# Kernel optimization log

Hardware: AMD Instinct MI355X
Metric: run time of the kernel (lower is better)

The kernel has to match this reference:

```python
import jax, jax.numpy as jnp
import numpy as np

NH, NL, NPNT = 8, 4, 4          # heads, levels, points
NQ, BS, NK, D, DFFN = 100, 8, 18, 256, 1024
SPATIAL = np.array([[92, 92], [46, 46], [23, 23], [12, 12]], np.int32)
LEN_MEM = int((SPATIAL[:, 0] * SPATIAL[:, 1]).sum())  # 11253


def _layernorm(x, g, b):
    m = x.mean(-1, keepdims=True)
    v = ((x - m) ** 2).mean(-1, keepdims=True)
    return (x - m) / jnp.sqrt(v + 1e-5) * g + b


def _mha(xq, xk, xv, in_w, in_b, out_w, out_b):
    # torch nn.MultiheadAttention semantics, inputs (S, B, D)
    S, B, d = xq.shape
    dh = d // NH
    wq, wk, wv = jnp.split(in_w, 3, axis=0)
    bq, bk, bv = jnp.split(in_b, 3, axis=0)
    def proj(x, w, b):
        return (x @ w.T + b).reshape(x.shape[0], B, NH, dh).transpose(1, 2, 0, 3)
    q = proj(xq, wq, bq) * (1.0 / np.sqrt(dh))
    k = proj(xk, wk, bk)
    v = proj(xv, wv, bv)
    att = jax.nn.softmax(jnp.einsum('bhqd,bhkd->bhqk', q, k), axis=-1)
    o = jnp.einsum('bhqk,bhkd->bhqd', att, v).transpose(2, 0, 1, 3).reshape(S, B, d)
    return o @ out_w.T + out_b


def _bilinear(v_l, loc):
    # v_l: (bs,H,W,NH,dh); loc: (bs,Lq,NH,P,2) normalized [0,1]
    # matches F.grid_sample(align_corners=False, padding_mode='zeros')
    bs, H, W, nh, dh = v_l.shape
    x = loc[..., 0] * W - 0.5
    y = loc[..., 1] * H - 0.5
    x0 = jnp.floor(x); y0 = jnp.floor(y)
    lx = x - x0; ly = y - y0
    b_idx = jnp.arange(bs)[:, None, None, None]
    h_idx = jnp.arange(nh)[None, None, :, None]
    def corner(xa, ya, w):
        valid = (xa >= 0) & (xa < W) & (ya >= 0) & (ya < H)
        xi = jnp.clip(xa, 0, W - 1).astype(jnp.int32)
        yi = jnp.clip(ya, 0, H - 1).astype(jnp.int32)
        return v_l[b_idx, yi, xi, h_idx] * (w * valid)[..., None]
    return (corner(x0, y0, (1 - lx) * (1 - ly)) + corner(x0 + 1, y0, lx * (1 - ly))
            + corner(x0, y0 + 1, (1 - lx) * ly) + corner(x0 + 1, y0 + 1, lx * ly))


def _msda(q, rp, mem, pad_mask, ss, off_w, off_b, aw_w, aw_b, val_w, val_b, outp_w, outp_b):
    bs, Lq, d = q.shape
    dh = d // NH
    value = mem @ val_w.T + val_b
    value = jnp.where(pad_mask[..., None], 0.0, value).reshape(bs, -1, NH, dh)
    off = (q @ off_w.T + off_b).reshape(bs, Lq, NH, NL, NPNT, 2)
    aw = jax.nn.softmax((q @ aw_w.T + aw_b).reshape(bs, Lq, NH, NL * NPNT), -1)
    aw = aw.reshape(bs, Lq, NH, NL, NPNT)
    wh = jnp.asarray(ss[:, ::-1].copy(), jnp.float32)  # offset normalizer (W, H)
    loc = rp[:, :, None, :, None, :] + off / wh[None, None, None, :, None, :]
    out = jnp.zeros((bs, Lq, NH, dh), q.dtype)
    start = 0
    for l in range(NL):
        H, W = int(ss[l, 0]), int(ss[l, 1])
        v_l = value[:, start:start + H * W].reshape(bs, H, W, NH, dh)
        start += H * W
        samp = _bilinear(v_l, loc[:, :, :, l])          # (bs,Lq,NH,P,dh)
        out = out + (samp * aw[:, :, :, l, :, None]).sum(3)
    return out.reshape(bs, Lq, d) @ outp_w.T + outp_b


def _forward(tgt_pose, pos, ref_points, memory, w_in_w, w_in_b, w_out_w, w_out_b,
             a_in_w, a_in_b, a_out_w, a_out_b, off_w, off_b, aw_w, aw_b,
             val_w, val_b, outp_w, outp_b, wn_g, wn_b, an_g, an_b,
             n1_g, n1_b, n2_g, n2_b, l1_w, l1_b, l2_w, l2_b,
             spatial_shapes, level_start_index, padding_mask):
    ss = np.asarray(jax.device_get(spatial_shapes))
    nq, bs, nk, d = tgt_pose.shape
    # within-group self-attn over the nk keypoint tokens.
    # NOTE: with_pos_embed mutates tgt_pose in place in the torch code, so
    # q = k = v = tgt + pos and the residual also uses tgt + pos (faithful).
    t = tgt_pose + pos
    x = t.reshape(nq * bs, nk, d).transpose(1, 0, 2)   # (nk, nq*bs, d)
    a1 = _mha(x, x, x, w_in_w, w_in_b, w_out_w, w_out_b)
    t = _layernorm(t + a1.transpose(1, 0, 2).reshape(nq, bs, nk, d), wn_g, wn_b)
    # across-group self-attn over the nq groups
    x2 = t.reshape(nq, bs * nk, d)
    a2 = _mha(x2, x2, x2, a_in_w, a_in_b, a_out_w, a_out_b)
    t = _layernorm(t + a2.reshape(nq, bs, nk, d), an_g, an_b)
    # MSDeformAttn cross-attention (in-place pos add again, faithful)
    t = t + pos
    q = t.transpose(1, 0, 2, 3).reshape(bs, nq * nk, d)
    rp = jnp.swapaxes(ref_points, 0, 1)                # (bs, nq*nk, NL, 2)
    mem = jnp.swapaxes(memory, 0, 1)                   # (bs, LEN_MEM, d)
    c = _msda(q, rp, mem, padding_mask, ss, off_w, off_b, aw_w, aw_b,
              val_w, val_b, outp_w, outp_b)
    c = c.reshape(bs, nq, nk, d).transpose(1, 0, 2, 3)
    t = _layernorm(t + c, n1_g, n1_b)
    # FFN (dropout is identity in eval)
    h = jax.nn.relu(t @ l1_w.T + l1_b)
    return _layernorm(t + (h @ l2_w.T + l2_b), n2_g, n2_b)


def setup_inputs() -> dict:
    key = jax.random.key(0)
    ks = jax.random.split(key, 16)
    p = lambda k, shape: jax.random.normal(k, shape, jnp.float32) * 0.02
    lsi = np.concatenate([[0], np.cumsum(SPATIAL[:, 0] * SPATIAL[:, 1])[:-1]]).astype(np.int32)
    return {
        'tgt_pose': jax.random.normal(ks[0], (NQ, BS, NK, D), jnp.float32),
        'pos': jax.random.normal(ks[1], (NQ, BS, NK, D), jnp.float32),
        'ref_points': jax.random.uniform(ks[2], (NQ * NK, BS, NL, 2), jnp.float32),
        'memory': jax.random.normal(ks[3], (LEN_MEM, BS, D), jnp.float32),
        'w_in_w': p(ks[4], (3 * D, D)), 'w_in_b': jnp.zeros((3 * D,)),
        'w_out_w': p(ks[5], (D, D)), 'w_out_b': jnp.zeros((D,)),
        'a_in_w': p(ks[6], (3 * D, D)), 'a_in_b': jnp.zeros((3 * D,)),
        'a_out_w': p(ks[7], (D, D)), 'a_out_b': jnp.zeros((D,)),
        'off_w': p(ks[8], (NH * NL * NPNT * 2, D)),
        'off_b': jax.random.uniform(ks[9], (NH * NL * NPNT * 2,), jnp.float32, -2.0, 2.0),
        'aw_w': p(ks[10], (NH * NL * NPNT, D)), 'aw_b': jnp.zeros((NH * NL * NPNT,)),
        'val_w': p(ks[11], (D, D)), 'val_b': jnp.zeros((D,)),
        'outp_w': p(ks[12], (D, D)), 'outp_b': jnp.zeros((D,)),
        'wn_g': jnp.ones((D,)), 'wn_b': jnp.zeros((D,)),
        'an_g': jnp.ones((D,)), 'an_b': jnp.zeros((D,)),
        'n1_g': jnp.ones((D,)), 'n1_b': jnp.zeros((D,)),
        'n2_g': jnp.ones((D,)), 'n2_b': jnp.zeros((D,)),
        'l1_w': p(ks[13], (DFFN, D)), 'l1_b': jnp.zeros((DFFN,)),
        'l2_w': p(ks[14], (D, DFFN)), 'l2_b': jnp.zeros((D,)),
        'spatial_shapes': jnp.asarray(SPATIAL),
        'level_start_index': jnp.asarray(lsi),
        'padding_mask': jnp.zeros((BS, LEN_MEM), bool),
    }


def reference(tgt_pose, pos, ref_points, memory, w_in_w, w_in_b, w_out_w, w_out_b,
              a_in_w, a_in_b, a_out_w, a_out_b, off_w, off_b, aw_w, aw_b,
              val_w, val_b, outp_w, outp_b, wn_g, wn_b, an_g, an_b,
              n1_g, n1_b, n2_g, n2_b, l1_w, l1_b, l2_w, l2_b,
              spatial_shapes, level_start_index, padding_mask):
    return _forward(tgt_pose, pos, ref_points, memory, w_in_w, w_in_b, w_out_w, w_out_b,
                    a_in_w, a_in_b, a_out_w, a_out_b, off_w, off_b, aw_w, aw_b,
                    val_w, val_b, outp_w, outp_b, wn_g, wn_b, an_g, an_b,
                    n1_g, n1_b, n2_g, n2_b, l1_w, l1_b, l2_w, l2_b,
                    spatial_shapes, level_start_index, padding_mask)
```

## Files before the change

### kernel.cpp

```cpp
#include <hip/hip_runtime.h>
#include <math.h>

#define NH_ 8
#define D_ 256
#define NK_ 18
#define NQ_ 100
#define BS_ 8
#define LQ_ 1800
#define LEN_MEM_ 11253
#define NTOK_ 14400

typedef short bf16x8 __attribute__((ext_vector_type(8)));
typedef float f32x4 __attribute__((ext_vector_type(4)));
typedef unsigned short ushort;

__device__ inline ushort f2bf(float f) {
    unsigned int u = __builtin_bit_cast(unsigned int, f);
    unsigned int r = (u + 0x7fffu + ((u >> 16) & 1u)) >> 16;
    return (ushort)r;
}
__device__ inline float bf2f(unsigned int u16) {
    unsigned int i = u16 << 16;
    return __builtin_bit_cast(float, i);
}
__device__ inline int packbf2(float a, float b) {
    return (int)f2bf(a) | ((int)f2bf(b) << 16);
}

__global__ __launch_bounds__(256)
void wcvt_kernel(const float* s0, const float* s1, const float* s2, const float* s3,
                 const float* s4, const float* s5, const float* s6, const float* s7,
                 const float* s8, const float* s9, ushort* dst) {
    const int sizes[10] = {196608,65536,196608,65536,65536,32768,65536,65536,262144,262144};
    const int offs[10]  = {0,196608,262144,458752,524288,589824,622592,688128,753664,1015808};
    int ti = blockIdx.y;
    const float* s;
    switch (ti) {
        case 0: s = s0; break; case 1: s = s1; break; case 2: s = s2; break;
        case 3: s = s3; break; case 4: s = s4; break; case 5: s = s5; break;
        case 6: s = s6; break; case 7: s = s7; break; case 8: s = s8; break;
        default: s = s9; break;
    }
    int n = sizes[ti];
    int i = (blockIdx.x * 256 + threadIdx.x) * 8;
    if (i >= n) return;
    ushort* d = dst + offs[ti] + i;
    float4 f0 = *(const float4*)(s + i);
    float4 f1 = *(const float4*)(s + i + 4);
    int4 val;
    val.x = packbf2(f0.x, f0.y);
    val.y = packbf2(f0.z, f0.w);
    val.z = packbf2(f1.x, f1.y);
    val.w = packbf2(f1.z, f1.w);
    *(int4*)d = val;
}

__global__ __launch_bounds__(256)
void addcvt_kernel(const float* __restrict__ a, const float* __restrict__ b,
                   float* __restrict__ c, ushort* __restrict__ cbf, int n4) {
    int i = blockIdx.x * blockDim.x + threadIdx.x;
    if (i >= n4) return;
    float4 av = ((const float4*)a)[i];
    float4 bv = ((const float4*)b)[i];
    float4 cv;
    cv.x = av.x + bv.x; cv.y = av.y + bv.y; cv.z = av.z + bv.z; cv.w = av.w + bv.w;
    ((float4*)c)[i] = cv;
    uint2 p;
    p.x = (unsigned int)packbf2(cv.x, cv.y);
    p.y = (unsigned int)packbf2(cv.z, cv.w);
    *(uint2*)(cbf + (size_t)i * 4) = p;
}

template<int MODE, bool RELU, bool A_F32, bool OUT_BF16, int BN, int WAVES>
__global__ __launch_bounds__(WAVES * 64)
void gemmw_kernel(const void* __restrict__ Av, const ushort* __restrict__ W,
                  const float* __restrict__ bias, void* __restrict__ Cv,
                  int M, int N, const unsigned char* __restrict__ mask) {
    constexpr int K = 256;
    constexpr int NT = BN / 16;
    __shared__ ushort Ws[32 * BN * 8];
    const int tid = threadIdx.x;
    const int m0 = blockIdx.x * (WAVES * 16);
    const int n0 = blockIdx.y * BN;

    for (int c = tid; c < 32 * BN; c += WAVES * 64) {
        int kc = c & 31, n = c >> 5;
        int dst = kc * BN + (n ^ (kc & 7));
        *(int4*)(Ws + dst * 8) = *(const int4*)(W + (long)(n0 + n) * K + kc * 8);
    }
    __syncthreads();

    const int wv = tid >> 6, lane = tid & 63, fr = lane & 15, hi = lane >> 4;
    const int wm0 = m0 + wv * 16;
    int gr = wm0 + fr;
    if (gr > M - 1) gr = M - 1;
    long arow;
    if (MODE == 2) {
        int b = gr / LQ_; int lq = gr - b * LQ_;
        int q = lq / NK_; int kk = lq - q * NK_;
        arow = (long)q * (BS_ * NK_) + b * NK_ + kk;
    } else {
        arow = gr;
    }

    f32x4 acc[NT];
#pragma unroll
    for (int t = 0; t < NT; ++t) acc[t] = f32x4{0.f, 0.f, 0.f, 0.f};

    if (A_F32) {
        const float* ap = (const float*)Av + arow * (long)K + hi * 8;
        float4 p0 = *(const float4*)ap;
        float4 p1 = *(const float4*)(ap + 4);
#pragma unroll
        for (int ks = 0; ks < 8; ++ks) {
            int4 v;
            v.x = packbf2(p0.x, p0.y); v.y = packbf2(p0.z, p0.w);
            v.z = packbf2(p1.x, p1.y); v.w = packbf2(p1.z, p1.w);
            bf16x8 cur = __builtin_bit_cast(bf16x8, v);
            if (ks < 7) {
                p0 = *(const float4*)(ap + (ks + 1) * 32);
                p1 = *(const float4*)(ap + (ks + 1) * 32 + 4);
            }
            const int kc = ks * 4 + hi;
            const ushort* wb = Ws + ((kc * BN) + (fr ^ (kc & 7))) * 8;
#pragma unroll
            for (int t = 0; t < NT; ++t) {
                bf16x8 wf = *(const bf16x8*)(wb + t * 128);
                acc[t] = __builtin_amdgcn_mfma_f32_16x16x32_bf16(cur, wf, acc[t], 0, 0, 0);
            }
        }
    } else {
        const ushort* ap = (const ushort*)Av + arow * (long)K + hi * 8;
        bf16x8 afrag = *(const bf16x8*)ap;
#pragma unroll
        for (int ks = 0; ks < 8; ++ks) {
            bf16x8 cur = afrag;
            if (ks < 7) afrag = *(const bf16x8*)(ap + (ks + 1) * 32);
            const int kc = ks * 4 + hi;
            const ushort* wb = Ws + ((kc * BN) + (fr ^ (kc & 7))) * 8;
#pragma unroll
            for (int t = 0; t < NT; ++t) {
                bf16x8 wf = *(const bf16x8*)(wb + t * 128);
                acc[t] = __builtin_amdgcn_mfma_f32_16x16x32_bf16(cur, wf, acc[t], 0, 0, 0);
            }
        }
    }

#pragma unroll
    for (int r = 0; r < 4; ++r) {
        int gm = wm0 + hi * 4 + r;
        if (gm >= M) continue;
        long orow = gm;
        bool zero = false;
        if (MODE == 1) {
            if (mask && mask[(size_t)(gm & 7) * LEN_MEM_ + (gm >> 3)]) zero = true;
        } else if (MODE == 3) {
            int b = gm / LQ_; int lq = gm - b * LQ_;
            int q = lq / NK_; int kk = lq - q * NK_;
            orow = (long)q * (BS_ * NK_) + b * NK_ + kk;
        }
#pragma unroll
        for (int t = 0; t < NT; ++t) {
            int gn = n0 + t * 16 + fr;
            float v = acc[t][r] + bias[gn];
            if (RELU) v = fmaxf(v, 0.f);
            if (zero) v = 0.f;
            if (OUT_BF16) ((ushort*)Cv)[orow * (long)N + gn] = f2bf(v);
            else ((float*)Cv)[orow * (long)N + gn] = v;
        }
    }
}

template<int MODE, bool RELU, bool A_F32, bool OUT_BF16>
__global__ __launch_bounds__(256)
void gemm_kernel(const void* __restrict__ Av, const ushort* __restrict__ W,
                 const float* __restrict__ bias, void* __restrict__ Cv,
                 int M, int N, int K, const unsigned char* __restrict__ mask) {
    constexpr int AST = 72;
    __shared__ ushort As[128 * AST];
    __shared__ ushort Bs[128 * AST];
    const int m0 = blockIdx.x * 128, n0 = blockIdx.y * 128;
    const int tid = threadIdx.x;
    const int w = tid >> 6, lane = tid & 63;
    const int wr = w >> 1, wc = w & 1;
    const int fr = lane & 15, hi = lane >> 4;
    f32x4 acc[4][4];
#pragma unroll
    for (int i = 0; i < 4; ++i)
#pragma unroll
        for (int j = 0; j < 4; ++j) acc[i][j] = f32x4{0.f, 0.f, 0.f, 0.f};

    const int srow = tid >> 1, shalf = tid & 1;
    long arow = 0;
    const bool avalid = (m0 + srow) < M;
    {
        int gr = m0 + srow;
        if (gr >= M) gr = M - 1;
        arow = gr;
    }

    for (int k0 = 0; k0 < K; k0 += 64) {
        ushort* ad = As + srow * AST + shalf * 32;
        if (avalid) {
            const ushort* ap = (const ushort*)Av + arow * (long)K + k0 + shalf * 32;
#pragma unroll
            for (int i = 0; i < 4; ++i) *(int4*)(ad + i * 8) = *(const int4*)(ap + i * 8);
        } else {
            int4 z = make_int4(0, 0, 0, 0);
#pragma unroll
            for (int i = 0; i < 4; ++i) *(int4*)(ad + i * 8) = z;
        }
        {
            const ushort* wp = W + (long)(n0 + srow) * K + k0 + shalf * 32;
            ushort* bd = Bs + srow * AST + shalf * 32;
#pragma unroll
            for (int i = 0; i < 4; ++i) *(int4*)(bd + i * 8) = *(const int4*)(wp + i * 8);
        }
        __syncthreads();
#pragma unroll
        for (int kb = 0; kb < 2; ++kb) {
            bf16x8 af[4], bfr[4];
#pragma unroll
            for (int i = 0; i < 4; ++i)
                af[i] = *(const bf16x8*)(As + (wr * 64 + i * 16 + fr) * AST + kb * 32 + hi * 8);
#pragma unroll
            for (int j = 0; j < 4; ++j)
                bfr[j] = *(const bf16x8*)(Bs + (wc * 64 + j * 16 + fr) * AST + kb * 32 + hi * 8);
#pragma unroll
            for (int i = 0; i < 4; ++i)
#pragma unroll
                for (int j = 0; j < 4; ++j)
                    acc[i][j] = __builtin_amdgcn_mfma_f32_16x16x32_bf16(af[i], bfr[j], acc[i][j], 0, 0, 0);
        }
        __syncthreads();
    }

#pragma unroll
    for (int i = 0; i < 4; ++i) {
#pragma unroll
        for (int r = 0; r < 4; ++r) {
            int gm = m0 + wr * 64 + i * 16 + hi * 4 + r;
            if (gm >= M) continue;
#pragma unroll
            for (int j = 0; j < 4; ++j) {
                int gn = n0 + wc * 64 + j * 16 + fr;
                float v = acc[i][j][r] + bias[gn];
                if (RELU) v = fmaxf(v, 0.f);
                if (OUT_BF16) ((ushort*)Cv)[(long)gm * N + gn] = f2bf(v);
                else ((float*)Cv)[(long)gm * N + gn] = v;
            }
        }
    }
}

template<int S, int SP, int HPB>
__global__ __launch_bounds__(256)
void mattn_kernel(const ushort* __restrict__ qkv, ushort* __restrict__ outb,
                  int rsG, int rsS) {
    constexpr int SPk = ((SP + 31) / 32) * 32;
    constexpr int KST = 40;
    constexpr int PST = SPk + 8;
    constexpr int NT = SP / 16;
    constexpr int NB = HPB * NT;
    constexpr int HB = 8 / HPB;
    __shared__ ushort KsA[HPB * SP * KST];
    __shared__ ushort VtA[HPB * 32 * PST];
    __shared__ ushort PA [HPB * SP * PST];

    const int tid = threadIdx.x;
    const int g = blockIdx.x / HB;
    const int hbase = (blockIdx.x % HB) * HPB;

    for (int idx = tid; idx < HPB * S * 4; idx += 256) {
        int hh = idx / (S * 4); int rem = idx - hh * (S * 4);
        int j = rem >> 2, q = rem & 3;
        const ushort* base = qkv + ((size_t)g * rsG + (size_t)j * rsS) * 768 + (hbase + hh) * 32 + q * 8;
        uint4 kv = *(const uint4*)(base + 256);
        ushort* kd = KsA + hh * (SP * KST) + j * KST + q * 8;
        *(uint2*)kd = make_uint2(kv.x, kv.y);
        *(uint2*)(kd + 4) = make_uint2(kv.z, kv.w);
        uint4 vv = *(const uint4*)(base + 512);
        ushort* vt = VtA + hh * (32 * PST) + j;
        unsigned int uu[4] = {vv.x, vv.y, vv.z, vv.w};
#pragma unroll
        for (int e = 0; e < 4; ++e) {
            vt[(q * 8 + e * 2    ) * PST] = (ushort)(uu[e] & 0xffff);
            vt[(q * 8 + e * 2 + 1) * PST] = (ushort)(uu[e] >> 16);
        }
    }
    for (int idx = tid; idx < HPB * 32 * (SPk - S); idx += 256) {
        int hh = idx / (32 * (SPk - S)); int rem = idx - hh * (32 * (SPk - S));
        int d = rem / (SPk - S); int c = S + rem - d * (SPk - S);
        VtA[hh * 32 * PST + d * PST + c] = 0;
    }
    if constexpr (SPk > SP) {
        constexpr int PW = SPk - SP;
        for (int idx = tid; idx < HPB * SP * PW; idx += 256) {
            int hh = idx / (SP * PW); int rem = idx - hh * (SP * PW);
            int rrow = rem / PW; int c = SP + rem - rrow * PW;
            PA[hh * SP * PST + rrow * PST + c] = 0;
        }
    }
    __syncthreads();

    const int wv = tid >> 6, lane = tid & 63, fr = lane & 15, hi = lane >> 4;
    for (int band = wv; band < NB; band += 4) {
        const int hh = band / NT, mb = band - (band / NT) * NT;
        const int h = hbase + hh;
        const ushort* Ks = KsA + hh * (SP * KST);
        const ushort* Vt = VtA + hh * (32 * PST);
        ushort* P = PA + hh * (SP * PST);

        int sq = mb * 16 + fr; if (sq > S - 1) sq = S - 1;
        bf16x8 qf = *(const bf16x8*)(qkv + ((size_t)g * rsG + (size_t)sq * rsS) * 768 + h * 32 + hi * 8);
        f32x4 sc[NT];
#pragma unroll
        for (int t = 0; t < NT; ++t) {
            bf16x8 kf = *(const bf16x8*)(Ks + (t * 16 + fr) * KST + hi * 8);
            sc[t] = __builtin_amdgcn_mfma_f32_16x16x32_bf16(qf, kf, f32x4{0.f, 0.f, 0.f, 0.f}, 0, 0, 0);
        }
#pragma unroll
        for (int t = 0; t < NT; ++t) {
            bool valid = (t * 16 + fr) < S;
#pragma unroll
            for (int r = 0; r < 4; ++r)
                sc[t][r] = valid ? sc[t][r] * 0.17677669529663687f : -1e30f;
        }
#pragma unroll
        for (int r = 0; r < 4; ++r) {
            float m = sc[0][r];
#pragma unroll
            for (int t = 1; t < NT; ++t) m = fmaxf(m, sc[t][r]);
            m = fmaxf(m, __shfl_xor(m, 1)); m = fmaxf(m, __shfl_xor(m, 2));
            m = fmaxf(m, __shfl_xor(m, 4)); m = fmaxf(m, __shfl_xor(m, 8));
            float e[NT]; float sum = 0.f;
#pragma unroll
            for (int t = 0; t < NT; ++t) { e[t] = __expf(sc[t][r] - m); sum += e[t]; }
            sum += __shfl_xor(sum, 1); sum += __shfl_xor(sum, 2);
            sum += __shfl_xor(sum, 4); sum += __shfl_xor(sum, 8);
            float inv = 1.f / sum;
            int row = mb * 16 + hi * 4 + r;
#pragma unroll
            for (int t = 0; t < NT; ++t)
                P[row * PST + t * 16 + fr] = f2bf(e[t] * inv);
        }
        f32x4 o0 = {0.f, 0.f, 0.f, 0.f}, o1 = {0.f, 0.f, 0.f, 0.f};
#pragma unroll
        for (int kb = 0; kb < SPk / 32; ++kb) {
            bf16x8 pf = *(const bf16x8*)(P + (mb * 16 + fr) * PST + kb * 32 + hi * 8);
            bf16x8 v0 = *(const bf16x8*)(Vt + fr * PST + kb * 32 + hi * 8);
            bf16x8 v1 = *(const bf16x8*)(Vt + (16 + fr) * PST + kb * 32 + hi * 8);
            o0 = __builtin_amdgcn_mfma_f32_16x16x32_bf16(pf, v0, o0, 0, 0, 0);
            o1 = __builtin_amdgcn_mfma_f32_16x16x32_bf16(pf, v1, o1, 0, 0, 0);
        }
#pragma unroll
        for (int r = 0; r < 4; ++r) {
            int s = mb * 16 + hi * 4 + r;
            if (s < S) {
                size_t ob = ((size_t)g * rsG + (size_t)s * rsS) * 256 + h * 32;
                outb[ob + fr] = f2bf(o0[r]);
                outb[ob + 16 + fr] = f2bf(o1[r]);
            }
        }
    }
}

__global__ __launch_bounds__(256)
void addln_kernel(const float* __restrict__ base, const float* __restrict__ delta,
                  const float* __restrict__ gamma, const float* __restrict__ beta,
                  const float* __restrict__ pos,
                  float* __restrict__ out, ushort* __restrict__ obf, int M) {
    int row = blockIdx.x * 4 + (threadIdx.x >> 6);
    int lane = threadIdx.x & 63;
    if (row >= M) return;
    const float* pb = base + (size_t)row * 256;
    const float* pd = delta + (size_t)row * 256;
    float v[4]; float s = 0.f;
#pragma unroll
    for (int i = 0; i < 4; ++i) { int c = lane + i * 64; v[i] = pb[c] + pd[c]; s += v[i]; }
#pragma unroll
    for (int off = 32; off; off >>= 1) s += __shfl_xor(s, off);
    float mean = s * (1.f / 256.f);
    float var = 0.f;
#pragma unroll
    for (int i = 0; i < 4; ++i) { float d = v[i] - mean; var += d * d; }
#pragma unroll
    for (int off = 32; off; off >>= 1) var += __shfl_xor(var, off);
    var *= (1.f / 256.f);
    float rstd = rsqrtf(var + 1e-5f);
#pragma unroll
    for (int i = 0; i < 4; ++i) {
        int c = lane + i * 64;
        float o = (v[i] - mean) * rstd * gamma[c] + beta[c];
        if (pos) o += pos[(size_t)row * 256 + c];
        out[(size_t)row * 256 + c] = o;
        if (obf) obf[(size_t)row * 256 + c] = f2bf(o);
    }
}

__global__ __launch_bounds__(256)
void msda_kernel(const float* __restrict__ offb, const float* __restrict__ aw,
                 const ushort* __restrict__ val, const float* __restrict__ refp,
                 const int* __restrict__ spatial, const int* __restrict__ lsi,
                 ushort* __restrict__ samp) {
    int unit = blockIdx.x * 16 + (threadIdx.x >> 4);
    int lane = threadIdx.x & 15;
    int lbase = (threadIdx.x & 63) & 48;
    int h = unit & 7;
    int t = unit >> 3;
    int lq = t % LQ_;
    int b = t / LQ_;

    float logit = aw[((size_t)b * LQ_ + lq) * 128 + h * 16 + lane];
    float m = logit;
    m = fmaxf(m, __shfl_xor(m, 1)); m = fmaxf(m, __shfl_xor(m, 2));
    m = fmaxf(m, __shfl_xor(m, 4)); m = fmaxf(m, __shfl_xor(m, 8));
    float e = __expf(logit - m);
    float sum = e;
    sum += __shfl_xor(sum, 1); sum += __shfl_xor(sum, 2);
    sum += __shfl_xor(sum, 4); sum += __shfl_xor(sum, 8);
    float wnorm = e / sum;

    const float* offp = offb + ((size_t)b * LQ_ + lq) * 256 + h * 32;
    float2 myoff = ((const float2*)offp)[lane];

    float acc0 = 0.f, acc1 = 0.f;
#pragma unroll
    for (int lvl = 0; lvl < 4; ++lvl) {
        int H = spatial[lvl * 2], W = spatial[lvl * 2 + 1];
        int st = lsi[lvl];
        float rpx = refp[(((size_t)lq * BS_ + b) * 4 + lvl) * 2 + 0];
        float rpy = refp[(((size_t)lq * BS_ + b) * 4 + lvl) * 2 + 1];
        const ushort* vb = val + ((size_t)st * 8 + b) * 256 + h * 32 + lane * 2;
        float fW = (float)W, fH = (float)H;
#pragma unroll
        for (int p = 0; p < 4; ++p) {
            int pi = lvl * 4 + p;
            float ox = __shfl(myoff.x, lbase + pi);
            float oy = __shfl(myoff.y, lbase + pi);
            float wpt = __shfl(wnorm, lbase + pi);
            float x = rpx * fW + ox - 0.5f;
            float y = rpy * fH + oy - 0.5f;
            float x0f = floorf(x), y0f = floorf(y);
            float lx = x - x0f, ly = y - y0f;
            int x0 = (int)x0f, y0 = (int)y0f;
            int xc0 = min(max(x0, 0), W - 1), xc1 = min(max(x0 + 1, 0), W - 1);
            int yc0 = min(max(y0, 0), H - 1), yc1 = min(max(y0 + 1, 0), H - 1);
            float vx0 = (x0 >= 0 && x0 < W) ? 1.f : 0.f;
            float vx1 = (x0 >= -1 && x0 + 1 < W) ? 1.f : 0.f;
            float vy0 = (y0 >= 0 && y0 < H) ? 1.f : 0.f;
            float vy1 = (y0 >= -1 && y0 + 1 < H) ? 1.f : 0.f;
            float w00 = wpt * (1.f - lx) * (1.f - ly) * vx0 * vy0;
            float w10 = wpt * lx * (1.f - ly) * vx1 * vy0;
            float w01 = wpt * (1.f - lx) * ly * vx0 * vy1;
            float w11 = wpt * lx * ly * vx1 * vy1;
            unsigned int u00 = *(const unsigned int*)(vb + ((size_t)(yc0 * W + xc0) * 8) * 256);
            unsigned int u10 = *(const unsigned int*)(vb + ((size_t)(yc0 * W + xc1) * 8) * 256);
            unsigned int u01 = *(const unsigned int*)(vb + ((size_t)(yc1 * W + xc0) * 8) * 256);
            unsigned int u11 = *(const unsigned int*)(vb + ((size_t)(yc1 * W + xc1) * 8) * 256);
            acc0 += w00 * bf2f(u00 & 0xffff) + w10 * bf2f(u10 & 0xffff)
                  + w01 * bf2f(u01 & 0xffff) + w11 * bf2f(u11 & 0xffff);
            acc1 += w00 * bf2f(u00 >> 16) + w10 * bf2f(u10 >> 16)
                  + w01 * bf2f(u01 >> 16) + w11 * bf2f(u11 >> 16);
        }
    }
    size_t o = ((size_t)b * LQ_ + lq) * 256 + h * 32 + lane * 2;
    *(unsigned int*)(samp + o) = (unsigned int)packbf2(acc0, acc1);
}

extern "C" void kernel_launch(void* const* d_in, const int* in_sizes, int n_in,
                              void* d_out, int out_size, void* d_ws, size_t ws_size,
                              hipStream_t stream) {
    const float* tgt     = (const float*)d_in[0];
    const float* pos     = (const float*)d_in[1];
    const float* refp    = (const float*)d_in[2];
    const float* memory  = (const float*)d_in[3];
    const float* w_in_w  = (const float*)d_in[4];
    const float* w_in_b  = (const float*)d_in[5];
    const float* w_out_w = (const float*)d_in[6];
    const float* w_out_b = (const float*)d_in[7];
    const float* a_in_w  = (const float*)d_in[8];
    const float* a_in_b  = (const float*)d_in[9];
    const float* a_out_w = (const float*)d_in[10];
    const float* a_out_b = (const float*)d_in[11];
    const float* off_w   = (const float*)d_in[12];
    const float* off_b   = (const float*)d_in[13];
    const float* aw_w    = (const float*)d_in[14];
    const float* aw_b    = (const float*)d_in[15];
    const float* val_w   = (const float*)d_in[16];
    const float* val_b   = (const float*)d_in[17];
    const float* outp_w  = (const float*)d_in[18];
    const float* outp_b  = (const float*)d_in[19];
    const float* wn_g    = (const float*)d_in[20];
    const float* wn_b    = (const float*)d_in[21];
    const float* an_g    = (const float*)d_in[22];
    const float* an_b    = (const float*)d_in[23];
    const float* n1_g    = (const float*)d_in[24];
    const float* n1_b    = (const float*)d_in[25];
    const float* n2_g    = (const float*)d_in[26];
    const float* n2_b    = (const float*)d_in[27];
    const float* l1_w    = (const float*)d_in[28];
    const float* l1_b    = (const float*)d_in[29];
    const float* l2_w    = (const float*)d_in[30];
    const float* l2_b    = (const float*)d_in[31];
    const int*   spatial = (const int*)d_in[32];
    const int*   lsi     = (const int*)d_in[33];
    const unsigned char* pmask = (const unsigned char*)d_in[34];
    float* out = (float*)d_out;

    float*  T      = (float*)d_ws;
    ushort* Tbf    = (ushort*)(T + 3686400);
    ushort* B16    = Tbf + 3686400;
    ushort* CBbf   = B16 + 11059200;
    ushort* VALbf  = CBbf + 3686400;
    ushort* SAMPbf = VALbf + 23046144;
    ushort* Hbf    = SAMPbf + 3686400;
    ushort* WB     = Hbf + 14745600;
    float*  OFF    = (float*)(WB + 1277952);
    float*  AW     = OFF + 3686400;

    ushort* WB_win  = WB + 0;
    ushort* WB_wout = WB + 196608;
    ushort* WB_ain  = WB + 262144;
    ushort* WB_aout = WB + 458752;
    ushort* WB_off  = WB + 524288;
    ushort* WB_aw   = WB + 589824;
    ushort* WB_val  = WB + 622592;
    ushort* WB_outp = WB + 688128;
    ushort* WB_l1   = WB + 753664;
    ushort* WB_l2   = WB + 1015808;

    const int n4 = NTOK_ * 256 / 4;

    wcvt_kernel<<<dim3(128, 10), 256, 0, stream>>>(
        w_in_w, w_out_w, a_in_w, a_out_w, off_w, aw_w, val_w, outp_w, l1_w, l2_w, WB);
    addcvt_kernel<<<n4 / 256, 256, 0, stream>>>(tgt, pos, T, Tbf, n4);
    gemmw_kernel<0, false, false, true, 128, 4><<<dim3(225, 6), 256, 0, stream>>>(
        Tbf, WB_win, w_in_b, B16, NTOK_, 768, nullptr);
    mattn_kernel<18, 32, 4><<<800 * 2, 256, 0, stream>>>(B16, CBbf, 18, 1);
    gemmw_kernel<0, false, false, false, 128, 4><<<dim3(225, 2), 256, 0, stream>>>(
        CBbf, WB_wout, w_out_b, OFF, NTOK_, 256, nullptr);
    addln_kernel<<<NTOK_ / 4, 256, 0, stream>>>(T, OFF, wn_g, wn_b, nullptr, T, Tbf, NTOK_);
    gemmw_kernel<0, false, false, true, 128, 4><<<dim3(225, 6), 256, 0, stream>>>(
        Tbf, WB_ain, a_in_b, B16, NTOK_, 768, nullptr);
    mattn_kernel<100, 112, 1><<<144 * 8, 256, 0, stream>>>(B16, CBbf, 1, 144);
    gemmw_kernel<0, false, false, false, 128, 4><<<dim3(225, 2), 256, 0, stream>>>(
        CBbf, WB_aout, a_out_b, OFF, NTOK_, 256, nullptr);
    addln_kernel<<<NTOK_ / 4, 256, 0, stream>>>(T, OFF, an_g, an_b, pos, T, Tbf, NTOK_);
    gemmw_kernel<1, false, true, true, 256, 8><<<dim3(704, 1), 512, 0, stream>>>(
        memory, WB_val, val_b, VALbf, 90024, 256, pmask);
    gemmw_kernel<2, false, false, false, 128, 4><<<dim3(225, 2), 256, 0, stream>>>(
        Tbf, WB_off, off_b, OFF, NTOK_, 256, nullptr);
    gemmw_kernel<2, false, false, false, 128, 4><<<dim3(225, 1), 256, 0, stream>>>(
        Tbf, WB_aw, aw_b, AW, NTOK_, 128, nullptr);
    msda_kernel<<<NTOK_ * 8 / 16, 256, 0, stream>>>(OFF, AW, VALbf, refp, spatial, lsi, SAMPbf);
    gemmw_kernel<3, false, false, false, 128, 4><<<dim3(225, 2), 256, 0, stream>>>(
        SAMPbf, WB_outp, outp_b, OFF, NTOK_, 256, nullptr);
    addln_kernel<<<NTOK_ / 4, 256, 0, stream>>>(T, OFF, n1_g, n1_b, nullptr, T, Tbf, NTOK_);
    gemmw_kernel<0, true, false, true, 128, 4><<<dim3(225, 8), 256, 0, stream>>>(
        Tbf, WB_l1, l1_b, Hbf, NTOK_, 1024, nullptr);
    gemm_kernel<0, false, false, false><<<dim3(113, 2), 256, 0, stream>>>(
        Hbf, WB_l2, l2_b, OFF, NTOK_, 256, 1024, nullptr);
    addln_kernel<<<NTOK_ / 4, 256, 0, stream>>>(T, OFF, n2_g, n2_b, nullptr, out, nullptr, NTOK_);
}
```

Measured before the change: 377.1 us.

## Double per-wave M tile in weight-stationary GEMM and widen MSDA gather vectors

```diff
diff --git a/kernel.cpp b/kernel.cpp
--- a/kernel.cpp
+++ b/kernel.cpp
@@ -21,6 +21,14 @@
 }
 __device__ inline float bf2f(unsigned int u16) {
     unsigned int i = u16 << 16;
+    return __builtin_bit_cast(float, i);
+}
+__device__ inline float bf2f_hi(unsigned int u) {
+    unsigned int i = u & 0xffff0000u;
+    return __builtin_bit_cast(float, i);
+}
+__device__ inline float bf2f_lo(unsigned int u) {
+    unsigned int i = u << 16;
     return __builtin_bit_cast(float, i);
 }
 __device__ inline int packbf2(float a, float b) {
@@ -71,7 +79,7 @@
     *(uint2*)(cbf + (size_t)i * 4) = p;
 }
 
-template<int MODE, bool RELU, bool A_F32, bool OUT_BF16, int BN, int WAVES>
+template<int MODE, bool RELU, bool A_F32, bool OUT_BF16, int BN, int WAVES, int R>
 __global__ __launch_bounds__(WAVES * 64)
 void gemmw_kernel(const void* __restrict__ Av, const ushort* __restrict__ W,
                   const float* __restrict__ bias, void* __restrict__ Cv,
@@ -80,7 +88,7 @@
     constexpr int NT = BN / 16;
     __shared__ ushort Ws[32 * BN * 8];
     const int tid = threadIdx.x;
-    const int m0 = blockIdx.x * (WAVES * 16);
+    const int m0 = blockIdx.x * (WAVES * 16 * R);
     const int n0 = blockIdx.y * BN;
 
     for (int c = tid; c < 32 * BN; c += WAVES * 64) {
@@ -91,82 +99,112 @@
     __syncthreads();
 
     const int wv = tid >> 6, lane = tid & 63, fr = lane & 15, hi = lane >> 4;
-    const int wm0 = m0 + wv * 16;
-    int gr = wm0 + fr;
-    if (gr > M - 1) gr = M - 1;
-    long arow;
-    if (MODE == 2) {
-        int b = gr / LQ_; int lq = gr - b * LQ_;
-        int q = lq / NK_; int kk = lq - q * NK_;
-        arow = (long)q * (BS_ * NK_) + b * NK_ + kk;
-    } else {
-        arow = gr;
-    }
-
-    f32x4 acc[NT];
-#pragma unroll
-    for (int t = 0; t < NT; ++t) acc[t] = f32x4{0.f, 0.f, 0.f, 0.f};
+    const int wm0 = m0 + wv * (16 * R);
+    long arow[R];
+#pragma unroll
+    for (int r = 0; r < R; ++r) {
+        int gr = wm0 + r * 16 + fr;
+        if (gr > M - 1) gr = M - 1;
+        if (MODE == 2) {
+            int b = gr / LQ_; int lq = gr - b * LQ_;
+            int q = lq / NK_; int kk = lq - q * NK_;
+            arow[r] = (long)q * (BS_ * NK_) + b * NK_ + kk;
+        } else {
+            arow[r] = gr;
+        }
+    }
+
+    f32x4 acc[R][NT];
+#pragma unroll
+    for (int r = 0; r < R; ++r)
+#pragma unroll
+        for (int t = 0; t < NT; ++t) acc[r][t] = f32x4{0.f, 0.f, 0.f, 0.f};
 
     if (A_F32) {
-        const float* ap = (const float*)Av + arow * (long)K + hi * 8;
-        float4 p0 = *(const float4*)ap;
-        float4 p1 = *(const float4*)(ap + 4);
+        const float* ap[R];
+        float4 p0[R], p1[R];
+#pragma unroll
+        for (int r = 0; r < R; ++r) {
+            ap[r] = (const float*)Av + arow[r] * (long)K + hi * 8;
+            p0[r] = *(const float4*)ap[r];
+            p1[r] = *(const float4*)(ap[r] + 4);
+        }
 #pragma unroll
         for (int ks = 0; ks < 8; ++ks) {
-            int4 v;
-            v.x = packbf2(p0.x, p0.y); v.y = packbf2(p0.z, p0.w);
-            v.z = packbf2(p1.x, p1.y); v.w = packbf2(p1.z, p1.w);
-            bf16x8 cur = __builtin_bit_cast(bf16x8, v);
-            if (ks < 7) {
-                p0 = *(const float4*)(ap + (ks + 1) * 32);
-                p1 = *(const float4*)(ap + (ks + 1) * 32 + 4);
+            bf16x8 cur[R];
+#pragma unroll
+            for (int r = 0; r < R; ++r) {
+                int4 v;
+                v.x = packbf2(p0[r].x, p0[r].y); v.y = packbf2(p0[r].z, p0[r].w);
+                v.z = packbf2(p1[r].x, p1[r].y); v.w = packbf2(p1[r].z, p1[r].w);
+                cur[r] = __builtin_bit_cast(bf16x8, v);
+                if (ks < 7) {
+                    p0[r] = *(const float4*)(ap[r] + (ks + 1) * 32);
+                    p1[r] = *(const float4*)(ap[r] + (ks + 1) * 32 + 4);
+                }
             }
             const int kc = ks * 4 + hi;
             const ushort* wb = Ws + ((kc * BN) + (fr ^ (kc & 7))) * 8;
 #pragma unroll
             for (int t = 0; t < NT; ++t) {
                 bf16x8 wf = *(const bf16x8*)(wb + t * 128);
-                acc[t] = __builtin_amdgcn_mfma_f32_16x16x32_bf16(cur, wf, acc[t], 0, 0, 0);
+#pragma unroll
+                for (int r = 0; r < R; ++r)
+                    acc[r][t] = __builtin_amdgcn_mfma_f32_16x16x32_bf16(cur[r], wf, acc[r][t], 0, 0, 0);
             }
         }
     } else {
-        const ushort* ap = (const ushort*)Av + arow * (long)K + hi * 8;
-        bf16x8 afrag = *(const bf16x8*)ap;
+        const ushort* ap[R];
+        bf16x8 afrag[R];
+#pragma unroll
+        for (int r = 0; r < R; ++r) {
+            ap[r] = (const ushort*)Av + arow[r] * (long)K + hi * 8;
+            afrag[r] = *(const bf16x8*)ap[r];
+        }
 #pragma unroll
         for (int ks = 0; ks < 8; ++ks) {
-            bf16x8 cur = afrag;
-            if (ks < 7) afrag = *(const bf16x8*)(ap + (ks + 1) * 32);
+            bf16x8 cur[R];
+#pragma unroll
+            for (int r = 0; r < R; ++r) {
+                cur[r] = afrag[r];
+                if (ks < 7) afrag[r] = *(const bf16x8*)(ap[r] + (ks + 1) * 32);
+            }
             const int kc = ks * 4 + hi;
             const ushort* wb = Ws + ((kc * BN) + (fr ^ (kc & 7))) * 8;
 #pragma unroll
             for (int t = 0; t < NT; ++t) {
                 bf16x8 wf = *(const bf16x8*)(wb + t * 128);
-                acc[t] = __builtin_amdgcn_mfma_f32_16x16x32_bf16(cur, wf, acc[t], 0, 0, 0);
-            }
-        }
-    }
-
-#pragma unroll
-    for (int r = 0; r < 4; ++r) {
-        int gm = wm0 + hi * 4 + r;
-        if (gm >= M) continue;
-        long orow = gm;
-        bool zero = false;
-        if (MODE == 1) {
-            if (mask && mask[(size_t)(gm & 7) * LEN_MEM_ + (gm >> 3)]) zero = true;
-        } else if (MODE == 3) {
-            int b = gm / LQ_; int lq = gm - b * LQ_;
-            int q = lq / NK_; int kk = lq - q * NK_;
-            orow = (long)q * (BS_ * NK_) + b * NK_ + kk;
-        }
-#pragma unroll
-        for (int t = 0; t < NT; ++t) {
-            int gn = n0 + t * 16 + fr;
-            float v = acc[t][r] + bias[gn];
-            if (RELU) v = fmaxf(v, 0.f);
-            if (zero) v = 0.f;
-            if (OUT_BF16) ((ushort*)Cv)[orow * (long)N + gn] = f2bf(v);
-            else ((float*)Cv)[orow * (long)N + gn] = v;
+#pragma unroll
+                for (int r = 0; r < R; ++r)
+                    acc[r][t] = __builtin_amdgcn_mfma_f32_16x16x32_bf16(cur[r], wf, acc[r][t], 0, 0, 0);
+            }
+        }
+    }
+
+#pragma unroll
+    for (int r = 0; r < R; ++r) {
+#pragma unroll
+        for (int rr = 0; rr < 4; ++rr) {
+            int gm = wm0 + r * 16 + hi * 4 + rr;
+            if (gm >= M) continue;
+            long orow = gm;
+            bool zero = false;
+            if (MODE == 1) {
+                if (mask && mask[(size_t)(gm & 7) * LEN_MEM_ + (gm >> 3)]) zero = true;
+            } else if (MODE == 3) {
+                int b = gm / LQ_; int lq = gm - b * LQ_;
+                int q = lq / NK_; int kk = lq - q * NK_;
+                orow = (long)q * (BS_ * NK_) + b * NK_ + kk;
+            }
+#pragma unroll
+            for (int t = 0; t < NT; ++t) {
+                int gn = n0 + t * 16 + fr;
+                float v = acc[r][t][rr] + bias[gn];
+                if (RELU) v = fmaxf(v, 0.f);
+                if (zero) v = 0.f;
+                if (OUT_BF16) ((ushort*)Cv)[orow * (long)N + gn] = f2bf(v);
+                else ((float*)Cv)[orow * (long)N + gn] = v;
+            }
         }
     }
 }
@@ -403,42 +441,55 @@
                  const ushort* __restrict__ val, const float* __restrict__ refp,
                  const int* __restrict__ spatial, const int* __restrict__ lsi,
                  ushort* __restrict__ samp) {
-    int unit = blockIdx.x * 16 + (threadIdx.x >> 4);
-    int lane = threadIdx.x & 15;
-    int lbase = (threadIdx.x & 63) & 48;
-    int h = unit & 7;
-    int t = unit >> 3;
-    int lq = t % LQ_;
-    int b = t / LQ_;
-
-    float logit = aw[((size_t)b * LQ_ + lq) * 128 + h * 16 + lane];
-    float m = logit;
+    const int unit = blockIdx.x * 64 + (threadIdx.x >> 2);
+    const int lane4 = threadIdx.x & 3;
+    const int base = (threadIdx.x & 63) & 60;
+    const int h = unit & 7;
+    const int t = unit >> 3;
+    const int lq = t % LQ_;
+    const int b = t / LQ_;
+    const size_t row = (size_t)b * LQ_ + lq;
+
+    float4 lg = *(const float4*)(aw + row * 128 + h * 16 + lane4 * 4);
+    float m = fmaxf(fmaxf(lg.x, lg.y), fmaxf(lg.z, lg.w));
     m = fmaxf(m, __shfl_xor(m, 1)); m = fmaxf(m, __shfl_xor(m, 2));
-    m = fmaxf(m, __shfl_xor(m, 4)); m = fmaxf(m, __shfl_xor(m, 8));
-    float e = __expf(logit - m);
-    float sum = e;
-    sum += __shfl_xor(sum, 1); sum += __shfl_xor(sum, 2);
-    sum += __shfl_xor(sum, 4); sum += __shfl_xor(sum, 8);
-    float wnorm = e / sum;
-
-    const float* offp = offb + ((size_t)b * LQ_ + lq) * 256 + h * 32;
-    float2 myoff = ((const float2*)offp)[lane];
-
-    float acc0 = 0.f, acc1 = 0.f;
+    float4 e;
+    e.x = __expf(lg.x - m); e.y = __expf(lg.y - m);
+    e.z = __expf(lg.z - m); e.w = __expf(lg.w - m);
+    float s = e.x + e.y + e.z + e.w;
+    s += __shfl_xor(s, 1); s += __shfl_xor(s, 2);
+    float inv = 1.f / s;
+    float4 w4; w4.x = e.x * inv; w4.y = e.y * inv; w4.z = e.z * inv; w4.w = e.w * inv;
+
+    const float* offp = offb + row * 256 + h * 32;
+    float4 oA = *(const float4*)(offp + lane4 * 8);
+    float4 oB = *(const float4*)(offp + lane4 * 8 + 4);
+
+    float acc[8];
+#pragma unroll
+    for (int c = 0; c < 8; ++c) acc[c] = 0.f;
+
 #pragma unroll
     for (int lvl = 0; lvl < 4; ++lvl) {
         int H = spatial[lvl * 2], W = spatial[lvl * 2 + 1];
         int st = lsi[lvl];
         float rpx = refp[(((size_t)lq * BS_ + b) * 4 + lvl) * 2 + 0];
         float rpy = refp[(((size_t)lq * BS_ + b) * 4 + lvl) * 2 + 1];
-        const ushort* vb = val + ((size_t)st * 8 + b) * 256 + h * 32 + lane * 2;
+        const ushort* vb = val + ((size_t)st * 8 + b) * 256 + h * 32 + lane4 * 8;
         float fW = (float)W, fH = (float)H;
 #pragma unroll
         for (int p = 0; p < 4; ++p) {
-            int pi = lvl * 4 + p;
-            float ox = __shfl(myoff.x, lbase + pi);
-            float oy = __shfl(myoff.y, lbase + pi);
-            float wpt = __shfl(wnorm, lbase + pi);
+            const int pi = lvl * 4 + p;
+            const int j = pi >> 2, q = pi & 3;
+            float ox_, oy_, wp_;
+            if (q == 0)      { ox_ = oA.x; oy_ = oA.y; wp_ = w4.x; }
+            else if (q == 1) { ox_ = oA.z; oy_ = oA.w; wp_ = w4.y; }
+            else if (q == 2) { ox_ = oB.x; oy_ = oB.y; wp_ = w4.z; }
+            else             { ox_ = oB.z; oy_ = oB.w; wp_ = w4.w; }
+            float ox  = __shfl(ox_, base + j);
+            float oy  = __shfl(oy_, base + j);
+            float wpt = __shfl(wp_, base + j);
+
             float x = rpx * fW + ox - 0.5f;
             float y = rpy * fH + oy - 0.5f;
             float x0f = floorf(x), y0f = floorf(y);
@@ -454,18 +505,30 @@
             float w10 = wpt * lx * (1.f - ly) * vx1 * vy0;
             float w01 = wpt * (1.f - lx) * ly * vx0 * vy1;
             float w11 = wpt * lx * ly * vx1 * vy1;
-            unsigned int u00 = *(const unsigned int*)(vb + ((size_t)(yc0 * W + xc0) * 8) * 256);
-            unsigned int u10 = *(const unsigned int*)(vb + ((size_t)(yc0 * W + xc1) * 8) * 256);
-            unsigned int u01 = *(const unsigned int*)(vb + ((size_t)(yc1 * W + xc0) * 8) * 256);
-            unsigned int u11 = *(const unsigned int*)(vb + ((size_t)(yc1 * W + xc1) * 8) * 256);
-            acc0 += w00 * bf2f(u00 & 0xffff) + w10 * bf2f(u10 & 0xffff)
-                  + w01 * bf2f(u01 & 0xffff) + w11 * bf2f(u11 & 0xffff);
-            acc1 += w00 * bf2f(u00 >> 16) + w10 * bf2f(u10 >> 16)
-                  + w01 * bf2f(u01 >> 16) + w11 * bf2f(u11 >> 16);
-        }
-    }
-    size_t o = ((size_t)b * LQ_ + lq) * 256 + h * 32 + lane * 2;
-    *(unsigned int*)(samp + o) = (unsigned int)packbf2(acc0, acc1);
+            uint4 u00 = *(const uint4*)(vb + (size_t)(yc0 * W + xc0) * 2048);
+            uint4 u10 = *(const uint4*)(vb + (size_t)(yc0 * W + xc1) * 2048);
+            uint4 u01 = *(const uint4*)(vb + (size_t)(yc1 * W + xc0) * 2048);
+            uint4 u11 = *(const uint4*)(vb + (size_t)(yc1 * W + xc1) * 2048);
+            const unsigned int* a00 = (const unsigned int*)&u00;
+            const unsigned int* a10 = (const unsigned int*)&u10;
+            const unsigned int* a01 = (const unsigned int*)&u01;
+            const unsigned int* a11 = (const unsigned int*)&u11;
+#pragma unroll
+            for (int k = 0; k < 4; ++k) {
+                acc[2 * k]     += w00 * bf2f_lo(a00[k]) + w10 * bf2f_lo(a10[k])
+                                + w01 * bf2f_lo(a01[k]) + w11 * bf2f_lo(a11[k]);
+                acc[2 * k + 1] += w00 * bf2f_hi(a00[k]) + w10 * bf2f_hi(a10[k])
+                                + w01 * bf2f_hi(a01[k]) + w11 * bf2f_hi(a11[k]);
+            }
+        }
+    }
+    size_t o = row * 256 + h * 32 + lane4 * 8;
+    uint4 pk;
+    pk.x = (unsigned int)packbf2(acc[0], acc[1]);
+    pk.y = (unsigned int)packbf2(acc[2], acc[3]);
+    pk.z = (unsigned int)packbf2(acc[4], acc[5]);
+    pk.w = (unsigned int)packbf2(acc[6], acc[7]);
+    *(uint4*)(samp + o) = pk;
 }
 
 extern "C" void kernel_launch(void* const* d_in, const int* in_sizes, int n_in,
@@ -535,29 +598,29 @@
     wcvt_kernel<<<dim3(128, 10), 256, 0, stream>>>(
         w_in_w, w_out_w, a_in_w, a_out_w, off_w, aw_w, val_w, outp_w, l1_w, l2_w, WB);
     addcvt_kernel<<<n4 / 256, 256, 0, stream>>>(tgt, pos, T, Tbf, n4);
-    gemmw_kernel<0, false, false, true, 128, 4><<<dim3(225, 6), 256, 0, stream>>>(
+    gemmw_kernel<0, false, false, true, 128, 4, 2><<<dim3(113, 6), 256, 0, stream>>>(
         Tbf, WB_win, w_in_b, B16, NTOK_, 768, nullptr);
     mattn_kernel<18, 32, 4><<<800 * 2, 256, 0, stream>>>(B16, CBbf, 18, 1);
-    gemmw_kernel<0, false, false, false, 128, 4><<<dim3(225, 2), 256, 0, stream>>>(
+    gemmw_kernel<0, false, false, false, 128, 4, 2><<<dim3(113, 2), 256, 0, stream>>>(
         CBbf, WB_wout, w_out_b, OFF, NTOK_, 256, nullptr);
     addln_kernel<<<NTOK_ / 4, 256, 0, stream>>>(T, OFF, wn_g, wn_b, nullptr, T, Tbf, NTOK_);
-    gemmw_kernel<0, false, false, true, 128, 4><<<dim3(225, 6), 256, 0, stream>>>(
+    gemmw_kernel<0, false, false, true, 128, 4, 2><<<dim3(113, 6), 256, 0, stream>>>(
         Tbf, WB_ain, a_in_b, B16, NTOK_, 768, nullptr);
     mattn_kernel<100, 112, 1><<<144 * 8, 256, 0, stream>>>(B16, CBbf, 1, 144);
-    gemmw_kernel<0, false, false, false, 128, 4><<<dim3(225, 2), 256, 0, stream>>>(
+    gemmw_kernel<0, false, false, false, 128, 4, 2><<<dim3(113, 2), 256, 0, stream>>>(
         CBbf, WB_aout, a_out_b, OFF, NTOK_, 256, nullptr);
     addln_kernel<<<NTOK_ / 4, 256, 0, stream>>>(T, OFF, an_g, an_b, pos, T, Tbf, NTOK_);
-    gemmw_kernel<1, false, true, true, 256, 8><<<dim3(704, 1), 512, 0, stream>>>(
+    gemmw_kernel<1, false, true, true, 256, 8, 2><<<dim3(352, 1), 512, 0, stream>>>(
         memory, WB_val, val_b, VALbf, 90024, 256, pmask);
-    gemmw_kernel<2, false, false, false, 128, 4><<<dim3(225, 2), 256, 0, stream>>>(
+    gemmw_kernel<2, false, false, false, 128, 4, 2><<<dim3(113, 2), 256, 0, stream>>>(
         Tbf, WB_off, off_b, OFF, NTOK_, 256, nullptr);
-    gemmw_kernel<2, false, false, false, 128, 4><<<dim3(225, 1), 256, 0, stream>>>(
+    gemmw_kernel<2, false, false, false, 128, 4, 2><<<dim3(113, 1), 256, 0, stream>>>(
         Tbf, WB_aw, aw_b, AW, NTOK_, 128, nullptr);
-    msda_kernel<<<NTOK_ * 8 / 16, 256, 0, stream>>>(OFF, AW, VALbf, refp, spatial, lsi, SAMPbf);
-    gemmw_kernel<3, false, false, false, 128, 4><<<dim3(225, 2), 256, 0, stream>>>(
+    msda_kernel<<<1800, 256, 0, stream>>>(OFF, AW, VALbf, refp, spatial, lsi, SAMPbf);
+    gemmw_kernel<3, false, false, false, 128, 4, 2><<<dim3(113, 2), 256, 0, stream>>>(
         SAMPbf, WB_outp, outp_b, OFF, NTOK_, 256, nullptr);
     addln_kernel<<<NTOK_ / 4, 256, 0, stream>>>(T, OFF, n1_g, n1_b, nullptr, T, Tbf, NTOK_);
-    gemmw_kernel<0, true, false, true, 128, 4><<<dim3(225, 8), 256, 0, stream>>>(
+    gemmw_kernel<0, true, false, true, 128, 4, 2><<<dim3(113, 8), 256, 0, stream>>>(
         Tbf, WB_l1, l1_b, Hbf, NTOK_, 1024, nullptr);
     gemm_kernel<0, false, false, false><<<dim3(113, 2), 256, 0, stream>>>(
         Hbf, WB_l2, l2_b, OFF, NTOK_, 256, 1024, nullptr);
```

Measured after the change: 375.1 us. No clear change (-0.5%).
